# Kernel optimization log

Measured on AMD Instinct MI355X. Metric: run time of the kernel, lower is better.

The kernel has to match this reference:

```python
import jax, jax.numpy as jnp
import numpy as np

N = 100000      # nodes
E = 1600000     # edges (avg degree 16)
IN_DIM = 16
D = 128         # layer width
H = 2           # attention heads (GATLayer default n_heads=2)
FC = 128
OUT_DIM = 4
L = 2           # len(layer_channels)-1 attention layers


def _gat_layer(x, src, dst, Wk, bk, Wq, bq, Wv, bv):
    # x: [N, D]; src/dst: [E]
    n = x.shape[0]
    dk = D // H
    k = (x @ Wk + bk).reshape(n, H, dk)
    q = (x @ Wq + bq).reshape(n, H, dk)
    v = (x @ Wv + bv).reshape(n, H, dk)
    # per-edge score: k_src . q_dst  -> [E, H]
    score = jnp.einsum('ehd,ehd->eh', k[src], q[dst])
    # edge softmax grouped by destination node
    smax = jax.ops.segment_max(score, dst, num_segments=n)          # [N, H]
    ex = jnp.exp(score - smax[dst])                                 # [E, H]
    denom = jax.ops.segment_sum(ex, dst, num_segments=n)           # [N, H]
    attn = ex / denom[dst]                                          # [E, H]
    # weighted scatter-sum of source values to destinations
    msg = v[src] * attn[:, :, None]                                 # [E, H, dk]
    res = jax.ops.segment_sum(msg, dst, num_segments=n)             # [N, H, dk]
    return res.reshape(n, D)


def setup_inputs() -> dict:
    key = jax.random.key(0)
    ks = jax.random.split(key, 24)
    def lin(k, fin, fout):
        w = jax.random.normal(k, (fin, fout), jnp.float32) * (1.0 / np.sqrt(fin))
        return w
    inp = {}
    inp['x'] = jax.random.normal(ks[0], (N, IN_DIM), jnp.float32)
    inp['src'] = jax.random.randint(ks[1], (E,), 0, N, jnp.int32)
    inp['dst'] = jax.random.randint(ks[2], (E,), 0, N, jnp.int32)
    inp['fc0_w'] = lin(ks[3], IN_DIM, D)
    inp['fc0_b'] = jnp.zeros((D,), jnp.float32)
    inp['Wk'] = jnp.stack([lin(ks[4 + i], D, D) for i in range(L)])
    inp['bk'] = jnp.zeros((L, D), jnp.float32)
    inp['Wq'] = jnp.stack([lin(ks[6 + i], D, D) for i in range(L)])
    inp['bq'] = jnp.zeros((L, D), jnp.float32)
    inp['Wv'] = jnp.stack([lin(ks[8 + i], D, D) for i in range(L)])
    inp['bv'] = jnp.zeros((L, D), jnp.float32)
    inp['ws_w'] = jnp.stack([lin(ks[10 + i], D, D) for i in range(L)])
    inp['ws_b'] = jnp.zeros((L, D), jnp.float32)
    inp['fc1_w'] = lin(ks[12], D, FC)
    inp['fc1_b'] = jnp.zeros((FC,), jnp.float32)
    inp['fc2_w'] = lin(ks[13], FC, OUT_DIM)
    inp['fc2_b'] = jnp.zeros((OUT_DIM,), jnp.float32)
    return inp


def reference(x, src, dst, fc0_w, fc0_b, Wk, bk, Wq, bq, Wv, bv, ws_w, ws_b, fc1_w, fc1_b, fc2_w, fc2_b):
    h = x @ fc0_w + fc0_b                                           # [N, D]
    for i in range(L):
        h = (h @ ws_w[i] + ws_b[i]) + _gat_layer(h, src, dst, Wk[i], bk[i], Wq[i], bq[i], Wv[i], bv[i])
        if i != L - 1:
            h = jax.nn.gelu(h)
    h = jax.nn.gelu(h @ fc1_w + fc1_b)                              # fc_channels > 0 branch
    return h @ fc2_w + fc2_b                                        # [N, OUT_DIM]
```

## Files before the change

### kernel.cpp

```cpp
#include <hip/hip_runtime.h>
#include <math.h>


typedef _Float16 f16x8 __attribute__((ext_vector_type(8)));
typedef _Float16 h2 __attribute__((ext_vector_type(2)));
typedef float f32x4 __attribute__((ext_vector_type(4)));

__device__ __forceinline__ ushort f2h(float x) {
    union { _Float16 h; ushort u; } v;
    v.h = (_Float16)x;
    return v.u;
}
__device__ __forceinline__ float h2f(ushort u) {
    union { ushort u; _Float16 h; } v;
    v.u = u;
    return (float)v.h;
}

__device__ __forceinline__ float gelu_f(float x) {
    float x3 = x * x * x;
    return 0.5f * x * (1.f + tanhf(0.7978845608028654f * (x + 0.044715f * x3)));
}

__device__ __forceinline__ h2 pk2(float a, float b) {
    return __builtin_bit_cast(h2, __builtin_amdgcn_cvt_pkrtz(a, b));
}

__global__ void k_zero(int* __restrict__ p, int n) {
    int i = blockIdx.x * blockDim.x + threadIdx.x;
    if (i < n) p[i] = 0;
}

__global__ void k_hist(const int* __restrict__ dst, int* __restrict__ deg,
                       int* __restrict__ rank, int e) {
    int i = blockIdx.x * blockDim.x + threadIdx.x;
    if (i < e) rank[i] = atomicAdd(&deg[dst[i]], 1);
}

__global__ __launch_bounds__(256) void k_part(const int* __restrict__ deg,
                                              int* __restrict__ pre,
                                              int* __restrict__ bsum, int n) {
    __shared__ int lds[256];
    int t = threadIdx.x;
    int base = blockIdx.x * 1024 + t * 4;
    int d0 = 0, d1 = 0, d2 = 0, d3 = 0;
    if (base + 3 < n) {
        int4 d = *(const int4*)&deg[base];
        d0 = d.x; d1 = d.y; d2 = d.z; d3 = d.w;
    } else {
        if (base + 0 < n) d0 = deg[base + 0];
        if (base + 1 < n) d1 = deg[base + 1];
        if (base + 2 < n) d2 = deg[base + 2];
        if (base + 3 < n) d3 = deg[base + 3];
    }
    int s0 = d0, s1 = s0 + d1, s2 = s1 + d2, s3 = s2 + d3;
    lds[t] = s3;
    __syncthreads();
    for (int off = 1; off < 256; off <<= 1) {
        int v = (t >= off) ? lds[t - off] : 0;
        __syncthreads();
        lds[t] += v;
        __syncthreads();
    }
    int excl = lds[t] - s3;
    if (base + 0 < n) pre[base + 0] = excl;
    if (base + 1 < n) pre[base + 1] = excl + s0;
    if (base + 2 < n) pre[base + 2] = excl + s1;
    if (base + 3 < n) pre[base + 3] = excl + s2;
    if (t == 255) bsum[blockIdx.x] = lds[255];
}

__global__ void k_scanb(int* __restrict__ bsum, int nb) {
    __shared__ int lds[128];
    int t = threadIdx.x;
    int v = (t < nb) ? bsum[t] : 0;
    lds[t] = v;
    __syncthreads();
    for (int off = 1; off < 128; off <<= 1) {
        int u = (t >= off) ? lds[t - off] : 0;
        __syncthreads();
        lds[t] += u;
        __syncthreads();
    }
    if (t < nb) bsum[t] = lds[t] - v;
}

__global__ __launch_bounds__(256) void k_add(int* __restrict__ rowp,
                                             const int* __restrict__ bsum, int n,
                                             int e) {
    int t = threadIdx.x;
    int base = blockIdx.x * 1024 + t * 4;
    int off = bsum[blockIdx.x];
#pragma unroll
    for (int j = 0; j < 4; ++j) {
        int i = base + j;
        if (i < n) rowp[i] += off;
    }
    if (blockIdx.x == 0 && t == 0) rowp[n] = e;
}

__global__ void k_scatter(const int* __restrict__ src, const int* __restrict__ dst,
                          const int* __restrict__ rank, const int* __restrict__ rowp,
                          int* __restrict__ csrc, int e) {
    int i = blockIdx.x * blockDim.x + threadIdx.x;
    if (i < e) csrc[rowp[dst[i]] + rank[i]] = src[i];
}

__global__ void k_pack(const float* __restrict__ Wk, const float* __restrict__ Wq,
                       const float* __restrict__ Wv, const float* __restrict__ Ws,
                       const float* __restrict__ Wfc1, ushort* __restrict__ Wp) {
    int id = blockIdx.y;
    const float* src;
    if (id < 8) {
        int m = id & 3, layer = id >> 2;
        src = (m == 0) ? Wk : (m == 1) ? Wq : (m == 2) ? Wv : Ws;
        src += layer * 16384;
    } else {
        src = Wfc1;
    }
    int o = blockIdx.x * 256 + threadIdx.x;
    int j = o & 7, l = (o >> 3) & 63, nf = (o >> 9) & 7, kc = o >> 12;
    int row = kc * 32 + ((l >> 4) << 3) + j;
    int col = nf * 16 + (l & 15);
    Wp[id * 16384 + o] = f2h(src[row * 128 + col]);
}

__global__ __launch_bounds__(256) void k_fc0(const float* __restrict__ X,
                                             const float* __restrict__ W,
                                             const float* __restrict__ b,
                                             float* __restrict__ H, int n) {
    __shared__ float Ws[16 * 128];
    __shared__ float xs[2][16];
    int t = threadIdx.x;
#pragma unroll
    for (int i = 0; i < 8; ++i) Ws[t + i * 256] = W[t + i * 256];
    if (t < 32) {
        int nn = blockIdx.x * 2 + (t >> 4);
        xs[t >> 4][t & 15] = (nn < n) ? X[nn * 16 + (t & 15)] : 0.f;
    }
    __syncthreads();
    int nd = blockIdx.x * 2 + (t >> 7);
    if (nd < n) {
        int c = t & 127;
        float acc = b[c];
#pragma unroll
        for (int j = 0; j < 16; ++j) acc += xs[t >> 7][j] * Ws[j * 128 + c];
        H[nd * 128 + c] = acc;
    }
}

__global__ __launch_bounds__(256) void k_gemm_mfma(
    const float* __restrict__ A, int n, const ushort* __restrict__ Wp,
    const float* __restrict__ b0, void* __restrict__ o0,
    const float* __restrict__ b1, void* __restrict__ o1,
    const float* __restrict__ b2, void* __restrict__ o2,
    const float* __restrict__ b3, void* __restrict__ o3,
    int flags, int nmat) {
    __shared__ ushort As[64 * 128];
    char* Asb = (char*)As;
    int t = threadIdx.x;
    int rbase = blockIdx.x * 64;

#pragma unroll
    for (int i = 0; i < 8; ++i) {
        int f = t * 4 + i * 1024;
        int r = f >> 7, c = f & 127;
        float4 v = {0.f, 0.f, 0.f, 0.f};
        if (rbase + r < n) v = *(const float4*)&A[(size_t)(rbase + r) * 128 + c];
        ushort4 u;
        u.x = f2h(v.x); u.y = f2h(v.y); u.z = f2h(v.z); u.w = f2h(v.w);
        int byte = (r * 256 + c * 2) ^ ((r & 7) << 4);
        *(ushort4*)(Asb + byte) = u;
    }
    __syncthreads();

    int w = t >> 6, l = t & 63;
    int arow = w * 16 + (l & 15);
    int kq = l >> 4;

    f16x8 a[4];
#pragma unroll
    for (int kc = 0; kc < 4; ++kc) {
        int byte = (arow * 256 + kc * 64 + kq * 16) ^ ((arow & 7) << 4);
        a[kc] = *(const f16x8*)(Asb + byte);
    }

    for (int m = 0; m < nmat; ++m) {
        const float* bias; void* op;
        if (m == 0)      { bias = b0; op = o0; }
        else if (m == 1) { bias = b1; op = o1; }
        else if (m == 2) { bias = b2; op = o2; }
        else             { bias = b3; op = o3; }
        int isf16 = (flags >> m) & 1;
        int act   = (flags >> (8 + m)) & 1;
        const ushort* wb = Wp + m * 16384;

        f32x4 acc[8];
#pragma unroll
        for (int nf = 0; nf < 8; ++nf) acc[nf] = (f32x4){0.f, 0.f, 0.f, 0.f};

#pragma unroll
        for (int kc = 0; kc < 4; ++kc) {
#pragma unroll
            for (int nf = 0; nf < 8; ++nf) {
                f16x8 b = *(const f16x8*)(wb + (((kc * 8 + nf) * 64 + l) << 3));
                acc[nf] = __builtin_amdgcn_mfma_f32_16x16x32_f16(a[kc], b, acc[nf], 0, 0, 0);
            }
        }

#pragma unroll
        for (int nf = 0; nf < 8; ++nf) {
            int col = nf * 16 + (l & 15);
            float bia = bias[col];
#pragma unroll
            for (int r = 0; r < 4; ++r) {
                int row = rbase + w * 16 + (l >> 4) * 4 + r;
                if (row < n) {
                    float o = acc[nf][r] + bia;
                    if (act) o = gelu_f(o);
                    if (isf16) ((ushort*)op)[(size_t)row * 128 + col] = f2h(o);
                    else       ((float*)op)[(size_t)row * 128 + col] = o;
                }
            }
        }
    }
}

__global__ void k_edge_hf(const ushort* __restrict__ K, const ushort* __restrict__ Q,
                          const ushort* __restrict__ V, const int* __restrict__ rowp,
                          const int* __restrict__ csrc, float* __restrict__ H, int n,
                          int act) {
    int wid = (int)((blockIdx.x * blockDim.x + threadIdx.x) >> 6);
    int lane = threadIdx.x & 63;
    if (wid >= n) return;
    int qb = lane >> 4;
    int w8 = (lane & 15) * 8;
    int e0 = rowp[wid], e1 = rowp[wid + 1];

    uint4 qr = *(const uint4*)&Q[(size_t)wid * 128 + w8];
    h2 q0 = __builtin_bit_cast(h2, qr.x), q1 = __builtin_bit_cast(h2, qr.y);
    h2 q2 = __builtin_bit_cast(h2, qr.z), q3 = __builtin_bit_cast(h2, qr.w);

    float m = -1e30f, denom = 0.f;
    h2 hz = {(_Float16)0.f, (_Float16)0.f};
    h2 acc0 = hz, acc1 = hz, acc2 = hz, acc3 = hz;

    for (int eb = e0; eb < e1; eb += 64) {
        int cnt = min(64, e1 - eb);
        int sl = (eb + lane < e1) ? csrc[eb + lane] : 0;
        int jm = (cnt + 3) >> 2;
#pragma unroll 2
        for (int j = 0; j < jm; ++j) {
            int ei = 4 * j + qb;
            bool val = ei < cnt;
            int s = __shfl(sl, ei);
            uint4 kr = *(const uint4*)&K[(size_t)s * 128 + w8];
            float sc = __builtin_amdgcn_fdot2(__builtin_bit_cast(h2, kr.x), q0,
                       __builtin_amdgcn_fdot2(__builtin_bit_cast(h2, kr.y), q1,
                       __builtin_amdgcn_fdot2(__builtin_bit_cast(h2, kr.z), q2,
                       __builtin_amdgcn_fdot2(__builtin_bit_cast(h2, kr.w), q3,
                                              0.f, false), false), false), false);
            sc += __shfl_xor(sc, 1);
            sc += __shfl_xor(sc, 2);
            sc += __shfl_xor(sc, 4);
            uint4 vr = *(const uint4*)&V[(size_t)s * 128 + w8];
            float mn = val ? fmaxf(m, sc) : m;
            float ss = __expf(m - mn);
            float p = val ? __expf(sc - mn) : 0.f;
            denom = denom * ss + p;
            h2 hp = pk2(p, p);
            h2 hs = pk2(ss, ss);
            acc0 = __builtin_bit_cast(h2, vr.x) * hp + acc0 * hs;
            acc1 = __builtin_bit_cast(h2, vr.y) * hp + acc1 * hs;
            acc2 = __builtin_bit_cast(h2, vr.z) * hp + acc2 * hs;
            acc3 = __builtin_bit_cast(h2, vr.w) * hp + acc3 * hs;
            m = mn;
        }
    }

    float a[8];
    a[0] = (float)acc0.x; a[1] = (float)acc0.y;
    a[2] = (float)acc1.x; a[3] = (float)acc1.y;
    a[4] = (float)acc2.x; a[5] = (float)acc2.y;
    a[6] = (float)acc3.x; a[7] = (float)acc3.y;

#pragma unroll
    for (int dist = 16; dist <= 32; dist <<= 1) {
        float mo = __shfl_xor(m, dist);
        float dn = __shfl_xor(denom, dist);
        float ao[8];
#pragma unroll
        for (int i = 0; i < 8; ++i) ao[i] = __shfl_xor(a[i], dist);
        float mn = fmaxf(m, mo);
        float sA = __expf(m - mn), sB = __expf(mo - mn);
        denom = denom * sA + dn * sB;
#pragma unroll
        for (int i = 0; i < 8; ++i) a[i] = a[i] * sA + ao[i] * sB;
        m = mn;
    }

    if (lane < 16) {
        float inv = (denom > 0.f) ? 1.f / denom : 0.f;
        float* hp = &H[(size_t)wid * 128 + w8];
        float4 h0 = *(float4*)hp;
        float4 h1 = *(float4*)(hp + 4);
        float o0 = h0.x + a[0] * inv, o1 = h0.y + a[1] * inv;
        float o2 = h0.z + a[2] * inv, o3 = h0.w + a[3] * inv;
        float o4 = h1.x + a[4] * inv, o5 = h1.y + a[5] * inv;
        float o6 = h1.z + a[6] * inv, o7 = h1.w + a[7] * inv;
        if (act) {
            o0 = gelu_f(o0); o1 = gelu_f(o1); o2 = gelu_f(o2); o3 = gelu_f(o3);
            o4 = gelu_f(o4); o5 = gelu_f(o5); o6 = gelu_f(o6); o7 = gelu_f(o7);
        }
        float4 w0 = {o0, o1, o2, o3};
        float4 w1 = {o4, o5, o6, o7};
        *(float4*)hp = w0;
        *(float4*)(hp + 4) = w1;
    }
}

__global__ void k_fc2(const ushort* __restrict__ Hh, const float* __restrict__ W,
                      const float* __restrict__ b, float* __restrict__ out, int n) {
    int wid = (int)((blockIdx.x * blockDim.x + threadIdx.x) >> 6);
    int lane = threadIdx.x & 63;
    if (wid >= n) return;
    unsigned raw = *(const unsigned*)(Hh + (size_t)wid * 128 + lane * 2);
    float x0 = h2f((ushort)(raw & 0xffff)), x1 = h2f((ushort)(raw >> 16));
    float4 wA = *(const float4*)&W[(lane * 2) * 4];
    float4 wB = *(const float4*)&W[(lane * 2 + 1) * 4];
    float a0 = x0 * wA.x + x1 * wB.x;
    float a1 = x0 * wA.y + x1 * wB.y;
    float a2 = x0 * wA.z + x1 * wB.z;
    float a3 = x0 * wA.w + x1 * wB.w;
#pragma unroll
    for (int off = 1; off < 64; off <<= 1) {
        a0 += __shfl_xor(a0, off);
        a1 += __shfl_xor(a1, off);
        a2 += __shfl_xor(a2, off);
        a3 += __shfl_xor(a3, off);
    }
    if (lane < 4) {
        float v = (lane == 0) ? a0 : (lane == 1) ? a1 : (lane == 2) ? a2 : a3;
        out[(size_t)wid * 4 + lane] = v + b[lane];
    }
}

extern "C" void kernel_launch(void* const* d_in, const int* in_sizes, int n_in,
                              void* d_out, int out_size, void* d_ws, size_t ws_size,
                              hipStream_t stream) {
    const float* x     = (const float*)d_in[0];
    const int*   src   = (const int*)d_in[1];
    const int*   dst   = (const int*)d_in[2];
    const float* fc0_w = (const float*)d_in[3];
    const float* fc0_b = (const float*)d_in[4];
    const float* Wk    = (const float*)d_in[5];
    const float* bk    = (const float*)d_in[6];
    const float* Wq    = (const float*)d_in[7];
    const float* bq    = (const float*)d_in[8];
    const float* Wv    = (const float*)d_in[9];
    const float* bv    = (const float*)d_in[10];
    const float* ws_w  = (const float*)d_in[11];
    const float* ws_b  = (const float*)d_in[12];
    const float* fc1_w = (const float*)d_in[13];
    const float* fc1_b = (const float*)d_in[14];
    const float* fc2_w = (const float*)d_in[15];
    const float* fc2_b = (const float*)d_in[16];

    int n = in_sizes[0] / 16;
    int e = in_sizes[1];

    float*  hA  = (float*)d_ws;
    float*  hB  = hA + (size_t)n * 128;
    ushort* Kb  = (ushort*)(hB + (size_t)n * 128);
    ushort* Qb  = Kb + (size_t)n * 128;
    ushort* Vb  = Qb + (size_t)n * 128;
    ushort* Wp  = Vb + (size_t)n * 128;
    int* deg    = (int*)(Wp + 9 * 16384);
    int* rowp   = deg + n;
    int* csrc   = rowp + n + 1;
    int* rank   = csrc + e;
    int* bsum   = rank + e;

    int nb = (n + 1023) / 1024;

    k_zero<<<(n + 255) / 256, 256, 0, stream>>>(deg, n);
    k_hist<<<(e + 255) / 256, 256, 0, stream>>>(dst, deg, rank, e);
    k_part<<<nb, 256, 0, stream>>>(deg, rowp, bsum, n);
    k_scanb<<<1, 128, 0, stream>>>(bsum, nb);
    k_add<<<nb, 256, 0, stream>>>(rowp, bsum, n, e);
    k_scatter<<<(e + 255) / 256, 256, 0, stream>>>(src, dst, rank, rowp, csrc, e);

    k_pack<<<dim3(64, 9), 256, 0, stream>>>(Wk, Wq, Wv, ws_w, fc1_w, Wp);

    k_fc0<<<(n + 1) / 2, 256, 0, stream>>>(x, fc0_w, fc0_b, hA, n);

    int gx = (n + 63) / 64;
    k_gemm_mfma<<<gx, 256, 0, stream>>>(hA, n, Wp, bk, Kb, bq, Qb, bv, Vb, ws_b, hB,
                                        0x07, 4);
    k_edge_hf<<<(n + 3) / 4, 256, 0, stream>>>(Kb, Qb, Vb, rowp, csrc, hB, n, 1);
    k_gemm_mfma<<<gx, 256, 0, stream>>>(hB, n, Wp + 4 * 16384, bk + 128, Kb, bq + 128,
                                        Qb, bv + 128, Vb, ws_b + 128, hA, 0x07, 4);
    k_edge_hf<<<(n + 3) / 4, 256, 0, stream>>>(Kb, Qb, Vb, rowp, csrc, hA, n, 0);

    k_gemm_mfma<<<gx, 256, 0, stream>>>(hA, n, Wp + 8 * 16384, fc1_b, Kb, fc1_b, Kb,
                                        fc1_b, Kb, fc1_b, Kb, 0x101, 1);
    k_fc2<<<(n + 3) / 4, 256, 0, stream>>>(Kb, fc2_w, fc2_b, (float*)d_out, n);
}
```

Baseline: 590.7 us.

## Fuse fc2 projection into fc1 GEMM epilogue and streamline edge kernel

Folds the final 128-to-4 projection into the fc1 MFMA GEMM epilogue. GELU outputs are multiplied by fc2 weights and reduced across lanes, so the separate k_fc2 launch and the f16 intermediate round-trip through memory are gone. In the edge kernel, the per-edge validity checks move out of the main loop into a remainder step, and address math uses 32-bit offsets. The cross-lane merge now stays in packed half precision, lowering shuffle count at some precision cost. GELU switches from tanhf to an exp-based form, which is cheaper but can overflow to NaN for large inputs.

```diff
diff --git a/kernel.cpp b/kernel.cpp
--- a/kernel.cpp
+++ b/kernel.cpp
@@ -18,8 +18,9 @@
 }
 
 __device__ __forceinline__ float gelu_f(float x) {
-    float x3 = x * x * x;
-    return 0.5f * x * (1.f + tanhf(0.7978845608028654f * (x + 0.044715f * x3)));
+    float y = 0.7978845608028654f * (x + 0.044715f * x * x * x);
+    float t = __expf(2.f * y);
+    return x * t / (t + 1.f);
 }
 
 __device__ __forceinline__ h2 pk2(float a, float b) {
@@ -153,9 +154,10 @@
     const float* __restrict__ A, int n, const ushort* __restrict__ Wp,
     const float* __restrict__ b0, void* __restrict__ o0,
     const float* __restrict__ b1, void* __restrict__ o1,
-    const float* __restrict__ b2, void* __restrict__ o2,
+    const float* __restrict__ b2_, void* __restrict__ o2,
     const float* __restrict__ b3, void* __restrict__ o3,
-    int flags, int nmat) {
+    const float* __restrict__ W2, const float* __restrict__ bias2,
+    float* __restrict__ out2, int flags, int nmat) {
     __shared__ ushort As[64 * 128];
     char* Asb = (char*)As;
     int t = threadIdx.x;
@@ -185,11 +187,13 @@
         a[kc] = *(const f16x8*)(Asb + byte);
     }
 
+    int fuse = (flags >> 16) & 1;
+
     for (int m = 0; m < nmat; ++m) {
         const float* bias; void* op;
         if (m == 0)      { bias = b0; op = o0; }
         else if (m == 1) { bias = b1; op = o1; }
-        else if (m == 2) { bias = b2; op = o2; }
+        else if (m == 2) { bias = b2_; op = o2; }
         else             { bias = b3; op = o3; }
         int isf16 = (flags >> m) & 1;
         int act   = (flags >> (8 + m)) & 1;
@@ -208,18 +212,59 @@
             }
         }
 
-#pragma unroll
-        for (int nf = 0; nf < 8; ++nf) {
-            int col = nf * 16 + (l & 15);
-            float bia = bias[col];
-#pragma unroll
-            for (int r = 0; r < 4; ++r) {
-                int row = rbase + w * 16 + (l >> 4) * 4 + r;
-                if (row < n) {
-                    float o = acc[nf][r] + bia;
-                    if (act) o = gelu_f(o);
-                    if (isf16) ((ushort*)op)[(size_t)row * 128 + col] = f2h(o);
-                    else       ((float*)op)[(size_t)row * 128 + col] = o;
+        if (fuse) {
+            float pj[4][4];
+#pragma unroll
+            for (int r = 0; r < 4; ++r)
+#pragma unroll
+                for (int j = 0; j < 4; ++j) pj[r][j] = 0.f;
+#pragma unroll
+            for (int nf = 0; nf < 8; ++nf) {
+                int col = nf * 16 + (l & 15);
+                float4 w2v = *(const float4*)&W2[col * 4];
+                float bia = bias[col];
+#pragma unroll
+                for (int r = 0; r < 4; ++r) {
+                    float o = gelu_f(acc[nf][r] + bia);
+                    pj[r][0] += o * w2v.x;
+                    pj[r][1] += o * w2v.y;
+                    pj[r][2] += o * w2v.z;
+                    pj[r][3] += o * w2v.w;
+                }
+            }
+#pragma unroll
+            for (int off = 1; off < 16; off <<= 1)
+#pragma unroll
+                for (int r = 0; r < 4; ++r)
+#pragma unroll
+                    for (int j = 0; j < 4; ++j)
+                        pj[r][j] += __shfl_xor(pj[r][j], off);
+            int jj = l & 15;
+            if (jj < 4) {
+#pragma unroll
+                for (int r = 0; r < 4; ++r) {
+                    int row = rbase + w * 16 + (l >> 4) * 4 + r;
+                    if (row < n) {
+                        float v = (jj == 0) ? pj[r][0] : (jj == 1) ? pj[r][1]
+                                : (jj == 2) ? pj[r][2] : pj[r][3];
+                        out2[(size_t)row * 4 + jj] = v + bias2[jj];
+                    }
+                }
+            }
+        } else {
+#pragma unroll
+            for (int nf = 0; nf < 8; ++nf) {
+                int col = nf * 16 + (l & 15);
+                float bia = bias[col];
+#pragma unroll
+                for (int r = 0; r < 4; ++r) {
+                    int row = rbase + w * 16 + (l >> 4) * 4 + r;
+                    if (row < n) {
+                        float o = acc[nf][r] + bia;
+                        if (act) o = gelu_f(o);
+                        if (isf16) ((ushort*)op)[(size_t)row * 128 + col] = f2h(o);
+                        else       ((float*)op)[(size_t)row * 128 + col] = o;
+                    }
                 }
             }
         }
@@ -234,10 +279,10 @@
     int lane = threadIdx.x & 63;
     if (wid >= n) return;
     int qb = lane >> 4;
-    int w8 = (lane & 15) * 8;
+    unsigned fb = (lane & 15) * 8u;
     int e0 = rowp[wid], e1 = rowp[wid + 1];
 
-    uint4 qr = *(const uint4*)&Q[(size_t)wid * 128 + w8];
+    uint4 qr = *(const uint4*)(Q + (((unsigned)wid << 7) + fb));
     h2 q0 = __builtin_bit_cast(h2, qr.x), q1 = __builtin_bit_cast(h2, qr.y);
     h2 q2 = __builtin_bit_cast(h2, qr.z), q3 = __builtin_bit_cast(h2, qr.w);
 
@@ -248,13 +293,12 @@
     for (int eb = e0; eb < e1; eb += 64) {
         int cnt = min(64, e1 - eb);
         int sl = (eb + lane < e1) ? csrc[eb + lane] : 0;
-        int jm = (cnt + 3) >> 2;
+        int full = cnt >> 2;
 #pragma unroll 2
-        for (int j = 0; j < jm; ++j) {
-            int ei = 4 * j + qb;
-            bool val = ei < cnt;
-            int s = __shfl(sl, ei);
-            uint4 kr = *(const uint4*)&K[(size_t)s * 128 + w8];
+        for (int j = 0; j < full; ++j) {
+            int s = __shfl(sl, 4 * j + qb);
+            unsigned off = ((unsigned)s << 7) + fb;
+            uint4 kr = *(const uint4*)(K + off);
             float sc = __builtin_amdgcn_fdot2(__builtin_bit_cast(h2, kr.x), q0,
                        __builtin_amdgcn_fdot2(__builtin_bit_cast(h2, kr.y), q1,
                        __builtin_amdgcn_fdot2(__builtin_bit_cast(h2, kr.z), q2,
@@ -263,7 +307,34 @@
             sc += __shfl_xor(sc, 1);
             sc += __shfl_xor(sc, 2);
             sc += __shfl_xor(sc, 4);
-            uint4 vr = *(const uint4*)&V[(size_t)s * 128 + w8];
+            uint4 vr = *(const uint4*)(V + off);
+            float mn = fmaxf(m, sc);
+            float ss = __expf(m - mn);
+            float p = __expf(sc - mn);
+            denom = denom * ss + p;
+            h2 hp = pk2(p, p);
+            h2 hs = pk2(ss, ss);
+            acc0 = __builtin_bit_cast(h2, vr.x) * hp + acc0 * hs;
+            acc1 = __builtin_bit_cast(h2, vr.y) * hp + acc1 * hs;
+            acc2 = __builtin_bit_cast(h2, vr.z) * hp + acc2 * hs;
+            acc3 = __builtin_bit_cast(h2, vr.w) * hp + acc3 * hs;
+            m = mn;
+        }
+        int rem = cnt & 3;
+        if (rem) {
+            bool val = qb < rem;
+            int s = __shfl(sl, full * 4 + qb);
+            unsigned off = ((unsigned)s << 7) + fb;
+            uint4 kr = *(const uint4*)(K + off);
+            float sc = __builtin_amdgcn_fdot2(__builtin_bit_cast(h2, kr.x), q0,
+                       __builtin_amdgcn_fdot2(__builtin_bit_cast(h2, kr.y), q1,
+                       __builtin_amdgcn_fdot2(__builtin_bit_cast(h2, kr.z), q2,
+                       __builtin_amdgcn_fdot2(__builtin_bit_cast(h2, kr.w), q3,
+                                              0.f, false), false), false), false);
+            sc += __shfl_xor(sc, 1);
+            sc += __shfl_xor(sc, 2);
+            sc += __shfl_xor(sc, 4);
+            uint4 vr = *(const uint4*)(V + off);
             float mn = val ? fmaxf(m, sc) : m;
             float ss = __expf(m - mn);
             float p = val ? __expf(sc - mn) : 0.f;
@@ -278,36 +349,34 @@
         }
     }
 
-    float a[8];
-    a[0] = (float)acc0.x; a[1] = (float)acc0.y;
-    a[2] = (float)acc1.x; a[3] = (float)acc1.y;
-    a[4] = (float)acc2.x; a[5] = (float)acc2.y;
-    a[6] = (float)acc3.x; a[7] = (float)acc3.y;
-
 #pragma unroll
     for (int dist = 16; dist <= 32; dist <<= 1) {
         float mo = __shfl_xor(m, dist);
         float dn = __shfl_xor(denom, dist);
-        float ao[8];
-#pragma unroll
-        for (int i = 0; i < 8; ++i) ao[i] = __shfl_xor(a[i], dist);
+        unsigned w0 = __shfl_xor(__builtin_bit_cast(unsigned, acc0), dist);
+        unsigned w1 = __shfl_xor(__builtin_bit_cast(unsigned, acc1), dist);
+        unsigned w2 = __shfl_xor(__builtin_bit_cast(unsigned, acc2), dist);
+        unsigned w3 = __shfl_xor(__builtin_bit_cast(unsigned, acc3), dist);
         float mn = fmaxf(m, mo);
         float sA = __expf(m - mn), sB = __expf(mo - mn);
         denom = denom * sA + dn * sB;
-#pragma unroll
-        for (int i = 0; i < 8; ++i) a[i] = a[i] * sA + ao[i] * sB;
+        h2 hA = pk2(sA, sA), hB = pk2(sB, sB);
+        acc0 = acc0 * hA + __builtin_bit_cast(h2, w0) * hB;
+        acc1 = acc1 * hA + __builtin_bit_cast(h2, w1) * hB;
+        acc2 = acc2 * hA + __builtin_bit_cast(h2, w2) * hB;
+        acc3 = acc3 * hA + __builtin_bit_cast(h2, w3) * hB;
         m = mn;
     }
 
     if (lane < 16) {
         float inv = (denom > 0.f) ? 1.f / denom : 0.f;
-        float* hp = &H[(size_t)wid * 128 + w8];
+        float* hp = H + (((unsigned)wid << 7) + fb);
         float4 h0 = *(float4*)hp;
         float4 h1 = *(float4*)(hp + 4);
-        float o0 = h0.x + a[0] * inv, o1 = h0.y + a[1] * inv;
-        float o2 = h0.z + a[2] * inv, o3 = h0.w + a[3] * inv;
-        float o4 = h1.x + a[4] * inv, o5 = h1.y + a[5] * inv;
-        float o6 = h1.z + a[6] * inv, o7 = h1.w + a[7] * inv;
+        float o0 = h0.x + (float)acc0.x * inv, o1 = h0.y + (float)acc0.y * inv;
+        float o2 = h0.z + (float)acc1.x * inv, o3 = h0.w + (float)acc1.y * inv;
+        float o4 = h1.x + (float)acc2.x * inv, o5 = h1.y + (float)acc2.y * inv;
+        float o6 = h1.z + (float)acc3.x * inv, o7 = h1.w + (float)acc3.y * inv;
         if (act) {
             o0 = gelu_f(o0); o1 = gelu_f(o1); o2 = gelu_f(o2); o3 = gelu_f(o3);
             o4 = gelu_f(o4); o5 = gelu_f(o5); o6 = gelu_f(o6); o7 = gelu_f(o7);
@@ -316,32 +385,6 @@
         float4 w1 = {o4, o5, o6, o7};
         *(float4*)hp = w0;
         *(float4*)(hp + 4) = w1;
-    }
-}
-
-__global__ void k_fc2(const ushort* __restrict__ Hh, const float* __restrict__ W,
-                      const float* __restrict__ b, float* __restrict__ out, int n) {
-    int wid = (int)((blockIdx.x * blockDim.x + threadIdx.x) >> 6);
-    int lane = threadIdx.x & 63;
-    if (wid >= n) return;
-    unsigned raw = *(const unsigned*)(Hh + (size_t)wid * 128 + lane * 2);
-    float x0 = h2f((ushort)(raw & 0xffff)), x1 = h2f((ushort)(raw >> 16));
-    float4 wA = *(const float4*)&W[(lane * 2) * 4];
-    float4 wB = *(const float4*)&W[(lane * 2 + 1) * 4];
-    float a0 = x0 * wA.x + x1 * wB.x;
-    float a1 = x0 * wA.y + x1 * wB.y;
-    float a2 = x0 * wA.z + x1 * wB.z;
-    float a3 = x0 * wA.w + x1 * wB.w;
-#pragma unroll
-    for (int off = 1; off < 64; off <<= 1) {
-        a0 += __shfl_xor(a0, off);
-        a1 += __shfl_xor(a1, off);
-        a2 += __shfl_xor(a2, off);
-        a3 += __shfl_xor(a3, off);
-    }
-    if (lane < 4) {
-        float v = (lane == 0) ? a0 : (lane == 1) ? a1 : (lane == 2) ? a2 : a3;
-        out[(size_t)wid * 4 + lane] = v + b[lane];
     }
 }
 
@@ -396,13 +439,15 @@
 
     int gx = (n + 63) / 64;
     k_gemm_mfma<<<gx, 256, 0, stream>>>(hA, n, Wp, bk, Kb, bq, Qb, bv, Vb, ws_b, hB,
-                                        0x07, 4);
+                                        nullptr, nullptr, nullptr, 0x07, 4);
     k_edge_hf<<<(n + 3) / 4, 256, 0, stream>>>(Kb, Qb, Vb, rowp, csrc, hB, n, 1);
     k_gemm_mfma<<<gx, 256, 0, stream>>>(hB, n, Wp + 4 * 16384, bk + 128, Kb, bq + 128,
-                                        Qb, bv + 128, Vb, ws_b + 128, hA, 0x07, 4);
+                                        Qb, bv + 128, Vb, ws_b + 128, hA,
+                                        nullptr, nullptr, nullptr, 0x07, 4);
     k_edge_hf<<<(n + 3) / 4, 256, 0, stream>>>(Kb, Qb, Vb, rowp, csrc, hA, n, 0);
 
-    k_gemm_mfma<<<gx, 256, 0, stream>>>(hA, n, Wp + 8 * 16384, fc1_b, Kb, fc1_b, Kb,
-                                        fc1_b, Kb, fc1_b, Kb, 0x101, 1);
-    k_fc2<<<(n + 3) / 4, 256, 0, stream>>>(Kb, fc2_w, fc2_b, (float*)d_out, n);
-}
+    k_gemm_mfma<<<gx, 256, 0, stream>>>(hA, n, Wp + 8 * 16384, fc1_b, nullptr,
+                                        fc1_b, nullptr, fc1_b, nullptr, fc1_b,
+                                        nullptr, fc2_w, fc2_b, (float*)d_out,
+                                        0x10000, 1);
+}
```

Result: slower. 691.1 us (+17.0%).
